# Kernel tuning notes

Hardware: AMD Instinct MI355X
Metric: run time of the kernel (lower is better)

The kernel has to match this reference:

```python
import jax, jax.numpy as jnp
import numpy as np
from jax import lax

BETA = 0.1

def setup_inputs() -> dict:
    key = jax.random.key(0)
    k = jax.random.split(key, 6)
    B, T, H, V = 2, 1024, 1024, 64000
    return {
        "_input": jax.random.normal(k[0], (B, T, H), jnp.float32) * 0.02,
        "weight": jax.random.normal(k[1], (V, H), jnp.float32) * 0.02,
        "attention_mask": (jax.random.uniform(k[2], (B, T)) < 0.9).astype(jnp.float32),
        "rewards": jax.random.normal(k[3], (B,), jnp.float32),
        "ref_input": jax.random.normal(k[4], (B, T, H), jnp.float32) * 0.02,
        "ref_weight": jax.random.normal(k[5], (V, H), jnp.float32) * 0.02,
    }


def _grpo(log_probs, attention_mask, rewards, ref_log_probs, beta):
    # log_probs: [B,T,V]
    chosen = jnp.argmax(log_probs, axis=-1)  # [B,T] int
    tok_lp = jnp.take_along_axis(log_probs, chosen[..., None], axis=-1)[..., 0]  # [B,T]
    ref_tok_lp = lax.stop_gradient(
        jnp.take_along_axis(ref_log_probs, chosen[..., None], axis=-1)[..., 0]
    )
    adv = (rewards - rewards.mean()) / (jnp.std(rewards, ddof=1) + 1e-8)  # [B]
    ratio = jnp.exp(tok_lp - lax.stop_gradient(tok_lp))  # == 1 in fwd, grad-carrying
    policy_loss = -ratio * adv[:, None]
    d = ref_tok_lp - tok_lp
    kl = jnp.exp(d) - d - 1.0
    per_tok = (policy_loss + beta * kl) * attention_mask
    seqlen = jnp.clip(attention_mask.sum(axis=1), 1.0)
    loss = (per_tok.sum(axis=1) / seqlen).mean()
    metrics = (
        tok_lp.mean(),
        jnp.std(tok_lp, ddof=1),
        log_probs.mean(),
        (kl * attention_mask).sum(axis=1).mean() / attention_mask.sum(axis=1).mean(),
    )
    return loss, metrics


def reference(_input, weight, attention_mask, rewards, ref_input, ref_weight):
    logits = jnp.einsum("bth,vh->btv", _input, weight)
    log_probs = jax.nn.log_softmax(logits, axis=-1)
    ref_logits = jnp.einsum("bth,vh->btv", ref_input, ref_weight)
    ref_log_probs = lax.stop_gradient(jax.nn.log_softmax(ref_logits, axis=-1))
    loss, metrics = _grpo(log_probs, attention_mask, rewards, ref_log_probs, BETA)
    return (loss, *metrics)
```

## Files before the change

### kernel.cpp

```cpp
#include <hip/hip_runtime.h>
#include <math.h>

#define GRPO_BETA 0.1f

constexpr int BM = 128;
constexpr int BN = 256;
constexpr int BK = 32;

typedef __attribute__((ext_vector_type(4))) float   f32x4;
typedef __attribute__((ext_vector_type(8))) __bf16  bf16x8;

__device__ __forceinline__ float sexp_fast(float a) { return __expf(fminf(a, 0.f)); }
__device__ __forceinline__ float sexp(float a)      { return expf(fminf(a, 0.f)); }

__device__ __forceinline__ bf16x8 cvt8(float4 a, float4 b) {
  bf16x8 r;
  r[0] = (__bf16)a.x; r[1] = (__bf16)a.y; r[2] = (__bf16)a.z; r[3] = (__bf16)a.w;
  r[4] = (__bf16)b.x; r[5] = (__bf16)b.y; r[6] = (__bf16)b.z; r[7] = (__bf16)b.w;
  return r;
}

__device__ __forceinline__ void bar_lgkm() {
  asm volatile("s_waitcnt lgkmcnt(0)\n\ts_barrier" ::: "memory");
}

__global__ __launch_bounds__(256)
void cvt_bf16_kernel(const float* __restrict__ src, __bf16* __restrict__ dst,
                     long long n8)
{
  long long i = (long long)blockIdx.x * blockDim.x + threadIdx.x;
  const long long stride = (long long)gridDim.x * blockDim.x;
  for (; i < n8; i += stride) {
    const float4 a = *reinterpret_cast<const float4*>(src + i * 8);
    const float4 b = *reinterpret_cast<const float4*>(src + i * 8 + 4);
    *reinterpret_cast<bf16x8*>(dst + i * 8) = cvt8(a, b);
  }
}

template <bool POLICY, bool CVT>
__global__ __launch_bounds__(512, 4)
void mfma_gemm_reduce(const float* __restrict__ Af,
                      const __bf16* __restrict__ Ah,
                      const float* __restrict__ Wf,
                      const __bf16* __restrict__ Wh,
                      float* __restrict__ part,
                      int M, int K, int V, int NC, int NL, int gx)
{
  __shared__ __align__(16) unsigned short lds_a[BM * 64];
  __shared__ __align__(16) unsigned short lds_w[BN * 64];
  __shared__ __align__(16) float4 lds_red[BM * 4];

  const int tid  = threadIdx.x;
  const int lane = tid & 63;
  const int wave = tid >> 6;
  const int wm   = wave >> 2;
  const int wn   = wave & 3;
  const int l15  = lane & 15;
  const int q    = lane >> 4;

  const int nb  = gridDim.x;
  int wl = blockIdx.x;
  if ((nb & 7) == 0) wl = (wl & 7) * (nb >> 3) + (wl >> 3);
  const int bx    = wl % gx;
  const int chunk = wl / gx;
  const int row0  = bx * BM;

  const int t3 = tid & 3;
  const int r4 = tid >> 2;
  const int stw = ((t3 * 16) ^ ((r4 & 7) << 4));
  const int sta = r4 * 128 + stw;

  const int arow = min(row0 + r4, M - 1);
  const int aro  = arow * K + t3 * 8;

  const int swzr  = ((q * 16) ^ ((l15 & 7) << 4));
  const int aoff0 = (wm * 64 + l15) * 128 + swzr;
  const int woff0 = (wn * 64 + l15) * 128 + swzr;

  float rm = -INFINITY, rse = 0.f, rsum = 0.f;
  int   ridx = 0x7fffffff;

  const int NS = K / BK;

  for (int sub = 0; sub < NL; ++sub) {
    const int v0 = (chunk * NL + sub) * BN;
    if (v0 >= V) break;

    int wro[2];
#pragma unroll
    for (int i = 0; i < 2; ++i)
      wro[i] = min(v0 + r4 + 128 * i, V - 1) * K + t3 * 8;

    f32x4 acc[4][4];
#pragma unroll
    for (int i = 0; i < 4; ++i)
#pragma unroll
      for (int j = 0; j < 4; ++j) acc[i][j] = (f32x4){0.f, 0.f, 0.f, 0.f};

    float4 aF[2], wF[2][2];
    bf16x8 aH, wH[2];

    if constexpr (CVT) {
      aF[0] = *reinterpret_cast<const float4*>(Af + aro);
      aF[1] = *reinterpret_cast<const float4*>(Af + aro + 4);
#pragma unroll
      for (int i = 0; i < 2; ++i) {
        wF[i][0] = *reinterpret_cast<const float4*>(Wf + wro[i]);
        wF[i][1] = *reinterpret_cast<const float4*>(Wf + wro[i] + 4);
      }
      *reinterpret_cast<bf16x8*>(reinterpret_cast<char*>(lds_a) + sta) = cvt8(aF[0], aF[1]);
#pragma unroll
      for (int i = 0; i < 2; ++i)
        *reinterpret_cast<bf16x8*>(reinterpret_cast<char*>(lds_w) + (r4 + 128 * i) * 128 + stw) =
            cvt8(wF[i][0], wF[i][1]);
      if (NS > 1) {
        aF[0] = *reinterpret_cast<const float4*>(Af + aro + BK);
        aF[1] = *reinterpret_cast<const float4*>(Af + aro + BK + 4);
#pragma unroll
        for (int i = 0; i < 2; ++i) {
          wF[i][0] = *reinterpret_cast<const float4*>(Wf + wro[i] + BK);
          wF[i][1] = *reinterpret_cast<const float4*>(Wf + wro[i] + BK + 4);
        }
      }
    } else {
      aH = *reinterpret_cast<const bf16x8*>(Ah + aro);
#pragma unroll
      for (int i = 0; i < 2; ++i)
        wH[i] = *reinterpret_cast<const bf16x8*>(Wh + wro[i]);
      *reinterpret_cast<bf16x8*>(reinterpret_cast<char*>(lds_a) + sta) = aH;
#pragma unroll
      for (int i = 0; i < 2; ++i)
        *reinterpret_cast<bf16x8*>(reinterpret_cast<char*>(lds_w) + (r4 + 128 * i) * 128 + stw) = wH[i];
      if (NS > 1) {
        aH = *reinterpret_cast<const bf16x8*>(Ah + aro + BK);
#pragma unroll
        for (int i = 0; i < 2; ++i)
          wH[i] = *reinterpret_cast<const bf16x8*>(Wh + wro[i] + BK);
      }
    }
    bar_lgkm();

    for (int s = 0; s < NS; ++s) {
      const int p = (s & 1) << 6;

      bf16x8 afr[4];
#pragma unroll
      for (int f = 0; f < 4; ++f)
        afr[f] = *reinterpret_cast<const bf16x8*>(
            reinterpret_cast<const char*>(lds_a) + (aoff0 ^ p) + f * 2048);
      __builtin_amdgcn_s_setprio(1);
#pragma unroll
      for (int fn = 0; fn < 4; ++fn) {
        bf16x8 wfr = *reinterpret_cast<const bf16x8*>(
            reinterpret_cast<const char*>(lds_w) + (woff0 ^ p) + fn * 2048);
#pragma unroll
        for (int fm = 0; fm < 4; ++fm)
          acc[fm][fn] = __builtin_amdgcn_mfma_f32_16x16x32_bf16(
              afr[fm], wfr, acc[fm][fn], 0, 0, 0);
      }
      __builtin_amdgcn_s_setprio(0);

      if (s + 1 < NS) {
        const int p1 = ((s + 1) & 1) << 6;
        if constexpr (CVT) {
          *reinterpret_cast<bf16x8*>(reinterpret_cast<char*>(lds_a) + (sta ^ p1)) =
              cvt8(aF[0], aF[1]);
#pragma unroll
          for (int i = 0; i < 2; ++i)
            *reinterpret_cast<bf16x8*>(
                reinterpret_cast<char*>(lds_w) + (((r4 + 128 * i) * 128 + stw) ^ p1)) =
                cvt8(wF[i][0], wF[i][1]);
          if (s + 2 < NS) {
            const int kf = (s + 2) * BK;
            aF[0] = *reinterpret_cast<const float4*>(Af + aro + kf);
            aF[1] = *reinterpret_cast<const float4*>(Af + aro + kf + 4);
#pragma unroll
            for (int i = 0; i < 2; ++i) {
              wF[i][0] = *reinterpret_cast<const float4*>(Wf + wro[i] + kf);
              wF[i][1] = *reinterpret_cast<const float4*>(Wf + wro[i] + kf + 4);
            }
          }
        } else {
          *reinterpret_cast<bf16x8*>(reinterpret_cast<char*>(lds_a) + (sta ^ p1)) = aH;
#pragma unroll
          for (int i = 0; i < 2; ++i)
            *reinterpret_cast<bf16x8*>(
                reinterpret_cast<char*>(lds_w) + (((r4 + 128 * i) * 128 + stw) ^ p1)) = wH[i];
          if (s + 2 < NS) {
            const int kf = (s + 2) * BK;
            aH = *reinterpret_cast<const bf16x8*>(Ah + aro + kf);
#pragma unroll
            for (int i = 0; i < 2; ++i)
              wH[i] = *reinterpret_cast<const bf16x8*>(Wh + wro[i] + kf);
          }
        }
      }
      bar_lgkm();
    }

#pragma unroll
    for (int fm = 0; fm < 4; ++fm) {
#pragma unroll
      for (int reg = 0; reg < 4; ++reg) {
        float lm = -INFINITY;
#pragma unroll
        for (int fn = 0; fn < 4; ++fn) {
          const int v = v0 + wn * 64 + fn * 16 + l15;
          if (v < V) lm = fmaxf(lm, acc[fm][fn][reg]);
        }
#pragma unroll
        for (int d = 1; d < 16; d <<= 1) lm = fmaxf(lm, __shfl_xor(lm, d));
        float se = 0.f, sm = 0.f; int li = 0x7fffffff;
#pragma unroll
        for (int fn = 0; fn < 4; ++fn) {
          const int v = v0 + wn * 64 + fn * 16 + l15;
          if (v < V) {
            const float x = acc[fm][fn][reg];
            se += __expf(x - lm);
            sm += x;
            if (x == lm) li = min(li, v);
          }
        }
#pragma unroll
        for (int d = 1; d < 16; d <<= 1) {
          se += __shfl_xor(se, d);
          sm += __shfl_xor(sm, d);
          li  = min(li, __shfl_xor(li, d));
        }
        if (l15 == 0) {
          const int row = wm * 64 + fm * 16 + q * 4 + reg;
          lds_red[row * 4 + wn] = make_float4(lm, se, sm, __int_as_float(li));
        }
      }
    }
    __syncthreads();

    if (tid < BM) {
      float4 p = lds_red[tid * 4];
      float m = p.x, se = p.y, sm = p.z; int idx = __float_as_int(p.w);
#pragma unroll
      for (int j = 1; j < 4; ++j) {
        const float4 t = lds_red[tid * 4 + j];
        const int ti = __float_as_int(t.w);
        const float nm = fmaxf(m, t.x);
        se = se * sexp_fast(m - nm) + t.y * sexp_fast(t.x - nm);
        sm += t.z;
        if (t.x > m || (t.x == m && ti < idx)) idx = ti;
        m = nm;
      }
      const float nm = fmaxf(rm, m);
      rse = rse * sexp_fast(rm - nm) + se * sexp_fast(m - nm);
      rsum += sm;
      if (m > rm || (m == rm && idx < ridx)) ridx = idx;
      rm = nm;
    }
    __syncthreads();
  }

  if (tid < BM) {
    const int row = row0 + tid;
    if (row < M) {
      if (POLICY) {
        reinterpret_cast<float4*>(part)[(size_t)row * NC + chunk] =
            make_float4(rm, rse, rsum, __int_as_float(ridx));
      } else {
        reinterpret_cast<float2*>(part)[(size_t)row * NC + chunk] =
            make_float2(rm, rse);
      }
    }
  }
}

__global__ __launch_bounds__(256)
void combine_kernel(const float4* __restrict__ partP,
                    const float2* __restrict__ partR,
                    const float* __restrict__ refA,
                    const float* __restrict__ refW,
                    float4* __restrict__ rowtab,
                    int M, int K, int V, int NC)
{
  const int row = blockIdx.x;
  const int tid = threadIdx.x;

  __shared__ float redf[256];
  __shared__ int   redi[256];
  __shared__ float s_M, s_SE, s_SUM, s_Mr, s_SEr, s_dot;
  __shared__ int   s_idx;

  float m = -INFINITY, se = 0.f, sm = 0.f; int idx = 0x7fffffff;
  for (int i = tid; i < NC; i += 256) {
    float4 p = partP[(size_t)row * NC + i];
    int pi = __float_as_int(p.w);
    float nm = fmaxf(m, p.x);
    se = se * sexp(m - nm) + p.y * sexp(p.x - nm);
    if (p.x > m || (p.x == m && pi < idx)) idx = pi;
    m = nm;
    sm += p.z;
  }
  redf[tid] = m; redi[tid] = idx;
  __syncthreads();
  for (int s = 128; s > 0; s >>= 1) {
    if (tid < s) {
      float om = redf[tid + s]; int oi = redi[tid + s];
      if (om > redf[tid] || (om == redf[tid] && oi < redi[tid])) { redf[tid] = om; redi[tid] = oi; }
    }
    __syncthreads();
  }
  if (tid == 0) { s_M = redf[0]; s_idx = redi[0]; }
  __syncthreads();
  const float Mp = s_M; const int chosen = s_idx;

  float contrib = se * sexp(m - Mp);
  __syncthreads();
  redf[tid] = contrib; __syncthreads();
  for (int s = 128; s > 0; s >>= 1) { if (tid < s) redf[tid] += redf[tid + s]; __syncthreads(); }
  if (tid == 0) s_SE = redf[0];
  __syncthreads();
  redf[tid] = sm; __syncthreads();
  for (int s = 128; s > 0; s >>= 1) { if (tid < s) redf[tid] += redf[tid + s]; __syncthreads(); }
  if (tid == 0) s_SUM = redf[0];
  __syncthreads();

  float mr = -INFINITY, ser = 0.f;
  for (int i = tid; i < NC; i += 256) {
    float2 p = partR[(size_t)row * NC + i];
    float nm = fmaxf(mr, p.x);
    ser = ser * sexp(mr - nm) + p.y * sexp(p.x - nm);
    mr = nm;
  }
  redf[tid] = mr; __syncthreads();
  for (int s = 128; s > 0; s >>= 1) { if (tid < s) redf[tid] = fmaxf(redf[tid], redf[tid + s]); __syncthreads(); }
  if (tid == 0) s_Mr = redf[0];
  __syncthreads();
  const float Mr = s_Mr;
  float contribr = ser * sexp(mr - Mr);
  __syncthreads();
  redf[tid] = contribr; __syncthreads();
  for (int s = 128; s > 0; s >>= 1) { if (tid < s) redf[tid] += redf[tid + s]; __syncthreads(); }
  if (tid == 0) s_SEr = redf[0];
  __syncthreads();

  float dp = 0.f;
  const float* ar = refA + (size_t)row * K;
  const float* wr = refW + (size_t)chosen * K;
  for (int j = tid * 4; j < K; j += 256 * 4) {
    float4 x = *reinterpret_cast<const float4*>(ar + j);
    float4 y = *reinterpret_cast<const float4*>(wr + j);
    dp = fmaf(x.x, y.x, dp);
    dp = fmaf(x.y, y.y, dp);
    dp = fmaf(x.z, y.z, dp);
    dp = fmaf(x.w, y.w, dp);
  }
  __syncthreads();
  redf[tid] = dp; __syncthreads();
  for (int s = 128; s > 0; s >>= 1) { if (tid < s) redf[tid] += redf[tid + s]; __syncthreads(); }
  if (tid == 0) s_dot = redf[0];
  __syncthreads();

  if (tid == 0) {
    float lse     = Mp + logf(s_SE);
    float tok     = Mp - lse;
    float ref_lse = Mr + logf(s_SEr);
    float ref_tok = s_dot - ref_lse;
    float d  = ref_tok - tok;
    float kl = expm1f(d) - d;
    float rm3 = s_SUM / (float)V - lse;
    rowtab[row] = make_float4(tok, kl, rm3, 0.f);
  }
}

__global__ __launch_bounds__(256)
void final_kernel(const float4* __restrict__ rowtab,
                  const float* __restrict__ mask,
                  const float* __restrict__ rewards,
                  float* __restrict__ out,
                  int M, int B, int T)
{
  const int tid = threadIdx.x;
  __shared__ float redf[256];
  __shared__ float s_mean, s_m3, s_var;
  __shared__ float s_kl[16], s_cnt[16];

  float st = 0.f, sm3 = 0.f;
  for (int r = tid; r < M; r += 256) {
    float4 v = rowtab[r];
    st += v.x; sm3 += v.z;
  }
  redf[tid] = st; __syncthreads();
  for (int s = 128; s > 0; s >>= 1) { if (tid < s) redf[tid] += redf[tid + s]; __syncthreads(); }
  if (tid == 0) s_mean = redf[0] / (float)M;
  __syncthreads();
  redf[tid] = sm3; __syncthreads();
  for (int s = 128; s > 0; s >>= 1) { if (tid < s) redf[tid] += redf[tid + s]; __syncthreads(); }
  if (tid == 0) s_m3 = redf[0] / (float)M;
  __syncthreads();

  const float mean = s_mean;
  float sv = 0.f;
  for (int r = tid; r < M; r += 256) { float d = rowtab[r].x - mean; sv = fmaf(d, d, sv); }
  __syncthreads();
  redf[tid] = sv; __syncthreads();
  for (int s = 128; s > 0; s >>= 1) { if (tid < s) redf[tid] += redf[tid + s]; __syncthreads(); }
  if (tid == 0) s_var = redf[0];
  __syncthreads();

  const int nb = B < 16 ? B : 16;
  for (int b = 0; b < nb; ++b) {
    float lk = 0.f, lc = 0.f;
    for (int t = tid; t < T; t += 256) {
      int r = b * T + t;
      float mk = mask[r];
      lk = fmaf(rowtab[r].y, mk, lk);
      lc += mk;
    }
    __syncthreads();
    redf[tid] = lk; __syncthreads();
    for (int s = 128; s > 0; s >>= 1) { if (tid < s) redf[tid] += redf[tid + s]; __syncthreads(); }
    if (tid == 0) s_kl[b] = redf[0];
    __syncthreads();
    redf[tid] = lc; __syncthreads();
    for (int s = 128; s > 0; s >>= 1) { if (tid < s) redf[tid] += redf[tid + s]; __syncthreads(); }
    if (tid == 0) s_cnt[b] = redf[0];
    __syncthreads();
  }

  if (tid == 0) {
    float rmean = 0.f;
    for (int b = 0; b < B; ++b) rmean += rewards[b];
    rmean /= (float)B;
    float rv = 0.f;
    for (int b = 0; b < B; ++b) { float d = rewards[b] - rmean; rv += d * d; }
    float rstd = sqrtf(rv / (float)(B > 1 ? B - 1 : 1));

    float loss = 0.f, m4n = 0.f, m4d = 0.f;
    for (int b = 0; b < nb; ++b) {
      float adv  = (rewards[b] - rmean) / (rstd + 1e-8f);
      float cnt  = s_cnt[b];
      float seql = fmaxf(cnt, 1.0f);
      loss += (-adv * cnt + GRPO_BETA * s_kl[b]) / seql;
      m4n += s_kl[b];
      m4d += cnt;
    }
    loss /= (float)B;

    out[0] = loss;
    out[1] = s_mean;
    out[2] = sqrtf(s_var / (float)(M - 1));
    out[3] = s_m3;
    out[4] = m4n / m4d;
  }
}

extern "C" void kernel_launch(void* const* d_in, const int* in_sizes, int n_in,
                              void* d_out, int out_size, void* d_ws, size_t ws_size,
                              hipStream_t stream)
{
  if (n_in < 6) return;
  const float* A       = (const float*)d_in[0];
  const float* W       = (const float*)d_in[1];
  const float* mask    = (const float*)d_in[2];
  const float* rewards = (const float*)d_in[3];
  const float* rA      = (const float*)d_in[4];
  const float* rW      = (const float*)d_in[5];

  const int M = in_sizes[2];
  const int B = in_sizes[3];
  const int T = M / B;
  const int K = in_sizes[0] / M;
  const int V = in_sizes[1] / K;

  const int gx = (M + BM - 1) / BM;

  const size_t aBytes = (size_t)M * K * sizeof(__bf16);
  const size_t wBytes = (size_t)V * K * sizeof(__bf16);
  auto partBytes = [&](int nl) -> size_t {
    int nc = (V + BN * nl - 1) / (BN * nl);
    return (size_t)M * nc * 16 + (size_t)M * nc * 8 + (size_t)M * 16;
  };
  const bool canPrep =
      (K % 8 == 0) && (partBytes(1) + 2 * aBytes + 2 * wBytes <= ws_size);

  int NL = 1;
  if (!canPrep) {
    while (partBytes(NL) > ws_size && NL < 1024) NL <<= 1;
  }
  const int NC = (V + BN * NL - 1) / (BN * NL);

  float* partP  = (float*)d_ws;
  float* partR  = partP + (size_t)M * NC * 4;
  float* rowtab = partR + (size_t)M * NC * 2;

  dim3 g1(gx * NC), b1(512);

  if (canPrep) {
    __bf16* Ab  = (__bf16*)(rowtab + (size_t)M * 4);
    __bf16* rAb = Ab  + (size_t)M * K;
    __bf16* Wb  = rAb + (size_t)M * K;
    __bf16* rWb = Wb  + (size_t)V * K;

    const long long nA8 = (long long)M * K / 8;
    const long long nW8 = (long long)V * K / 8;
    cvt_bf16_kernel<<<dim3(512),  dim3(256), 0, stream>>>(A,  Ab,  nA8);
    cvt_bf16_kernel<<<dim3(512),  dim3(256), 0, stream>>>(rA, rAb, nA8);
    cvt_bf16_kernel<<<dim3(2048), dim3(256), 0, stream>>>(W,  Wb,  nW8);
    cvt_bf16_kernel<<<dim3(2048), dim3(256), 0, stream>>>(rW, rWb, nW8);

    mfma_gemm_reduce<true , false><<<g1, b1, 0, stream>>>(
        nullptr, Ab,  nullptr, Wb,  partP, M, K, V, NC, NL, gx);
    mfma_gemm_reduce<false, false><<<g1, b1, 0, stream>>>(
        nullptr, rAb, nullptr, rWb, partR, M, K, V, NC, NL, gx);
  } else {
    mfma_gemm_reduce<true , true><<<g1, b1, 0, stream>>>(
        A,  nullptr, W,  nullptr, partP, M, K, V, NC, NL, gx);
    mfma_gemm_reduce<false, true><<<g1, b1, 0, stream>>>(
        rA, nullptr, rW, nullptr, partR, M, K, V, NC, NL, gx);
  }

  combine_kernel<<<dim3(M), dim3(256), 0, stream>>>(
      (const float4*)partP, (const float2*)partR, rA, rW, (float4*)rowtab, M, K, V, NC);
  final_kernel<<<dim3(1), dim3(256), 0, stream>>>(
      (const float4*)rowtab, mask, rewards, (float*)d_out, M, B, T);
}
```

Measured before the change: 876.4 us.

## Shrink GEMM tile to 128x128 with 4 waves and specialize reduction paths

Changes the fused GEMM+softmax-reduce tile from 128x256 with 8 waves to 128x128 with 4 waves. Each wave still computes a 64x64 sub-tile, but blocks are smaller and twice as many, with less LDS per block for better occupancy and load balance. Also adds a FULL template that drops vocab bounds checks when V divides BN, skips sum/argmax work in the reference pass, and lets the workspace search pick a larger NL so the bf16 pre-conversion path can still fit. The smaller N tile lowers A-tile reuse per block and doubles the partial-result count the combine kernel must merge.

```diff
diff --git a/kernel.cpp b/kernel.cpp
--- a/kernel.cpp
+++ b/kernel.cpp
@@ -4,7 +4,7 @@
 #define GRPO_BETA 0.1f
 
 constexpr int BM = 128;
-constexpr int BN = 256;
+constexpr int BN = 128;
 constexpr int BK = 32;
 
 typedef __attribute__((ext_vector_type(4))) float   f32x4;
@@ -37,8 +37,8 @@
   }
 }
 
-template <bool POLICY, bool CVT>
-__global__ __launch_bounds__(512, 4)
+template <bool POLICY, bool CVT, bool FULL>
+__global__ __launch_bounds__(256, 4)
 void mfma_gemm_reduce(const float* __restrict__ Af,
                       const __bf16* __restrict__ Ah,
                       const float* __restrict__ Wf,
@@ -48,13 +48,13 @@
 {
   __shared__ __align__(16) unsigned short lds_a[BM * 64];
   __shared__ __align__(16) unsigned short lds_w[BN * 64];
-  __shared__ __align__(16) float4 lds_red[BM * 4];
+  __shared__ __align__(16) float4 lds_red[BM * 2];
 
   const int tid  = threadIdx.x;
   const int lane = tid & 63;
   const int wave = tid >> 6;
-  const int wm   = wave >> 2;
-  const int wn   = wave & 3;
+  const int wm   = wave >> 1;
+  const int wn   = wave & 1;
   const int l15  = lane & 15;
   const int q    = lane >> 4;
 
@@ -68,10 +68,9 @@
   const int t3 = tid & 3;
   const int r4 = tid >> 2;
   const int stw = ((t3 * 16) ^ ((r4 & 7) << 4));
-  const int sta = r4 * 128 + stw;
-
-  const int arow = min(row0 + r4, M - 1);
-  const int aro  = arow * K + t3 * 8;
+  int aro[2];
+#pragma unroll
+  for (int i = 0; i < 2; ++i) aro[i] = min(row0 + r4 + 64 * i, M - 1) * K + t3 * 8;
 
   const int swzr  = ((q * 16) ^ ((l15 & 7) << 4));
   const int aoff0 = (wm * 64 + l15) * 128 + swzr;
@@ -89,7 +88,7 @@
     int wro[2];
 #pragma unroll
     for (int i = 0; i < 2; ++i)
-      wro[i] = min(v0 + r4 + 128 * i, V - 1) * K + t3 * 8;
+      wro[i] = min(v0 + r4 + 64 * i, V - 1) * K + t3 * 8;
 
     f32x4 acc[4][4];
 #pragma unroll
@@ -97,45 +96,50 @@
 #pragma unroll
       for (int j = 0; j < 4; ++j) acc[i][j] = (f32x4){0.f, 0.f, 0.f, 0.f};
 
-    float4 aF[2], wF[2][2];
-    bf16x8 aH, wH[2];
+    float4 aF[2][2], wF[2][2];
+    bf16x8 aH[2], wH[2];
 
     if constexpr (CVT) {
-      aF[0] = *reinterpret_cast<const float4*>(Af + aro);
-      aF[1] = *reinterpret_cast<const float4*>(Af + aro + 4);
 #pragma unroll
       for (int i = 0; i < 2; ++i) {
+        aF[i][0] = *reinterpret_cast<const float4*>(Af + aro[i]);
+        aF[i][1] = *reinterpret_cast<const float4*>(Af + aro[i] + 4);
         wF[i][0] = *reinterpret_cast<const float4*>(Wf + wro[i]);
         wF[i][1] = *reinterpret_cast<const float4*>(Wf + wro[i] + 4);
       }
-      *reinterpret_cast<bf16x8*>(reinterpret_cast<char*>(lds_a) + sta) = cvt8(aF[0], aF[1]);
-#pragma unroll
-      for (int i = 0; i < 2; ++i)
-        *reinterpret_cast<bf16x8*>(reinterpret_cast<char*>(lds_w) + (r4 + 128 * i) * 128 + stw) =
+#pragma unroll
+      for (int i = 0; i < 2; ++i) {
+        *reinterpret_cast<bf16x8*>(reinterpret_cast<char*>(lds_a) + (r4 + 64 * i) * 128 + stw) =
+            cvt8(aF[i][0], aF[i][1]);
+        *reinterpret_cast<bf16x8*>(reinterpret_cast<char*>(lds_w) + (r4 + 64 * i) * 128 + stw) =
             cvt8(wF[i][0], wF[i][1]);
+      }
       if (NS > 1) {
-        aF[0] = *reinterpret_cast<const float4*>(Af + aro + BK);
-        aF[1] = *reinterpret_cast<const float4*>(Af + aro + BK + 4);
 #pragma unroll
         for (int i = 0; i < 2; ++i) {
+          aF[i][0] = *reinterpret_cast<const float4*>(Af + aro[i] + BK);
+          aF[i][1] = *reinterpret_cast<const float4*>(Af + aro[i] + BK + 4);
           wF[i][0] = *reinterpret_cast<const float4*>(Wf + wro[i] + BK);
           wF[i][1] = *reinterpret_cast<const float4*>(Wf + wro[i] + BK + 4);
         }
       }
     } else {
-      aH = *reinterpret_cast<const bf16x8*>(Ah + aro);
-#pragma unroll
-      for (int i = 0; i < 2; ++i)
+#pragma unroll
+      for (int i = 0; i < 2; ++i) {
+        aH[i] = *reinterpret_cast<const bf16x8*>(Ah + aro[i]);
         wH[i] = *reinterpret_cast<const bf16x8*>(Wh + wro[i]);
-      *reinterpret_cast<bf16x8*>(reinterpret_cast<char*>(lds_a) + sta) = aH;
-#pragma unroll
-      for (int i = 0; i < 2; ++i)
-        *reinterpret_cast<bf16x8*>(reinterpret_cast<char*>(lds_w) + (r4 + 128 * i) * 128 + stw) = wH[i];
+      }
+#pragma unroll
+      for (int i = 0; i < 2; ++i) {
+        *reinterpret_cast<bf16x8*>(reinterpret_cast<char*>(lds_a) + (r4 + 64 * i) * 128 + stw) = aH[i];
+        *reinterpret_cast<bf16x8*>(reinterpret_cast<char*>(lds_w) + (r4 + 64 * i) * 128 + stw) = wH[i];
+      }
       if (NS > 1) {
-        aH = *reinterpret_cast<const bf16x8*>(Ah + aro + BK);
-#pragma unroll
-        for (int i = 0; i < 2; ++i)
+#pragma unroll
+        for (int i = 0; i < 2; ++i) {
+          aH[i] = *reinterpret_cast<const bf16x8*>(Ah + aro[i] + BK);
           wH[i] = *reinterpret_cast<const bf16x8*>(Wh + wro[i] + BK);
+        }
       }
     }
     bar_lgkm();
@@ -163,35 +167,40 @@
       if (s + 1 < NS) {
         const int p1 = ((s + 1) & 1) << 6;
         if constexpr (CVT) {
-          *reinterpret_cast<bf16x8*>(reinterpret_cast<char*>(lds_a) + (sta ^ p1)) =
-              cvt8(aF[0], aF[1]);
-#pragma unroll
-          for (int i = 0; i < 2; ++i)
+#pragma unroll
+          for (int i = 0; i < 2; ++i) {
             *reinterpret_cast<bf16x8*>(
-                reinterpret_cast<char*>(lds_w) + (((r4 + 128 * i) * 128 + stw) ^ p1)) =
+                reinterpret_cast<char*>(lds_a) + (((r4 + 64 * i) * 128 + stw) ^ p1)) =
+                cvt8(aF[i][0], aF[i][1]);
+            *reinterpret_cast<bf16x8*>(
+                reinterpret_cast<char*>(lds_w) + (((r4 + 64 * i) * 128 + stw) ^ p1)) =
                 cvt8(wF[i][0], wF[i][1]);
+          }
           if (s + 2 < NS) {
             const int kf = (s + 2) * BK;
-            aF[0] = *reinterpret_cast<const float4*>(Af + aro + kf);
-            aF[1] = *reinterpret_cast<const float4*>(Af + aro + kf + 4);
 #pragma unroll
             for (int i = 0; i < 2; ++i) {
+              aF[i][0] = *reinterpret_cast<const float4*>(Af + aro[i] + kf);
+              aF[i][1] = *reinterpret_cast<const float4*>(Af + aro[i] + kf + 4);
               wF[i][0] = *reinterpret_cast<const float4*>(Wf + wro[i] + kf);
               wF[i][1] = *reinterpret_cast<const float4*>(Wf + wro[i] + kf + 4);
             }
           }
         } else {
-          *reinterpret_cast<bf16x8*>(reinterpret_cast<char*>(lds_a) + (sta ^ p1)) = aH;
-#pragma unroll
-          for (int i = 0; i < 2; ++i)
+#pragma unroll
+          for (int i = 0; i < 2; ++i) {
             *reinterpret_cast<bf16x8*>(
-                reinterpret_cast<char*>(lds_w) + (((r4 + 128 * i) * 128 + stw) ^ p1)) = wH[i];
+                reinterpret_cast<char*>(lds_a) + (((r4 + 64 * i) * 128 + stw) ^ p1)) = aH[i];
+            *reinterpret_cast<bf16x8*>(
+                reinterpret_cast<char*>(lds_w) + (((r4 + 64 * i) * 128 + stw) ^ p1)) = wH[i];
+          }
           if (s + 2 < NS) {
             const int kf = (s + 2) * BK;
-            aH = *reinterpret_cast<const bf16x8*>(Ah + aro + kf);
-#pragma unroll
-            for (int i = 0; i < 2; ++i)
+#pragma unroll
+            for (int i = 0; i < 2; ++i) {
+              aH[i] = *reinterpret_cast<const bf16x8*>(Ah + aro[i] + kf);
               wH[i] = *reinterpret_cast<const bf16x8*>(Wh + wro[i] + kf);
+            }
           }
         }
       }
@@ -205,8 +214,8 @@
         float lm = -INFINITY;
 #pragma unroll
         for (int fn = 0; fn < 4; ++fn) {
-          const int v = v0 + wn * 64 + fn * 16 + l15;
-          if (v < V) lm = fmaxf(lm, acc[fm][fn][reg]);
+          if (FULL || v0 + wn * 64 + fn * 16 + l15 < V)
+            lm = fmaxf(lm, acc[fm][fn][reg]);
         }
 #pragma unroll
         for (int d = 1; d < 16; d <<= 1) lm = fmaxf(lm, __shfl_xor(lm, d));
@@ -214,44 +223,51 @@
 #pragma unroll
         for (int fn = 0; fn < 4; ++fn) {
           const int v = v0 + wn * 64 + fn * 16 + l15;
-          if (v < V) {
+          if (FULL || v < V) {
             const float x = acc[fm][fn][reg];
             se += __expf(x - lm);
-            sm += x;
-            if (x == lm) li = min(li, v);
+            if constexpr (POLICY) {
+              sm += x;
+              if (x == lm) li = min(li, v);
+            }
           }
         }
 #pragma unroll
         for (int d = 1; d < 16; d <<= 1) {
           se += __shfl_xor(se, d);
-          sm += __shfl_xor(sm, d);
-          li  = min(li, __shfl_xor(li, d));
+          if constexpr (POLICY) {
+            sm += __shfl_xor(sm, d);
+            li  = min(li, __shfl_xor(li, d));
+          }
         }
         if (l15 == 0) {
           const int row = wm * 64 + fm * 16 + q * 4 + reg;
-          lds_red[row * 4 + wn] = make_float4(lm, se, sm, __int_as_float(li));
+          lds_red[row * 2 + wn] = make_float4(lm, se, sm, __int_as_float(li));
         }
       }
     }
     __syncthreads();
 
     if (tid < BM) {
-      float4 p = lds_red[tid * 4];
-      float m = p.x, se = p.y, sm = p.z; int idx = __float_as_int(p.w);
-#pragma unroll
-      for (int j = 1; j < 4; ++j) {
-        const float4 t = lds_red[tid * 4 + j];
-        const int ti = __float_as_int(t.w);
-        const float nm = fmaxf(m, t.x);
-        se = se * sexp_fast(m - nm) + t.y * sexp_fast(t.x - nm);
-        sm += t.z;
-        if (t.x > m || (t.x == m && ti < idx)) idx = ti;
+      float4 p0 = lds_red[tid * 2];
+      float4 p1 = lds_red[tid * 2 + 1];
+      float m = p0.x, se = p0.y, sm = p0.z; int idx = __float_as_int(p0.w);
+      {
+        const int ti = __float_as_int(p1.w);
+        const float nm = fmaxf(m, p1.x);
+        se = se * sexp_fast(m - nm) + p1.y * sexp_fast(p1.x - nm);
+        if constexpr (POLICY) {
+          sm += p1.z;
+          if (p1.x > m || (p1.x == m && ti < idx)) idx = ti;
+        }
         m = nm;
       }
       const float nm = fmaxf(rm, m);
       rse = rse * sexp_fast(rm - nm) + se * sexp_fast(m - nm);
-      rsum += sm;
-      if (m > rm || (m == rm && idx < ridx)) ridx = idx;
+      if constexpr (POLICY) {
+        rsum += sm;
+        if (m > rm || (m == rm && idx < ridx)) ridx = idx;
+      }
       rm = nm;
     }
     __syncthreads();
@@ -260,7 +276,7 @@
   if (tid < BM) {
     const int row = row0 + tid;
     if (row < M) {
-      if (POLICY) {
+      if constexpr (POLICY) {
         reinterpret_cast<float4*>(part)[(size_t)row * NC + chunk] =
             make_float4(rm, rse, rsum, __int_as_float(ridx));
       } else {
@@ -470,6 +486,7 @@
   const int V = in_sizes[1] / K;
 
   const int gx = (M + BM - 1) / BM;
+  const bool full = (V % BN) == 0;
 
   const size_t aBytes = (size_t)M * K * sizeof(__bf16);
   const size_t wBytes = (size_t)V * K * sizeof(__bf16);
@@ -477,11 +494,17 @@
     int nc = (V + BN * nl - 1) / (BN * nl);
     return (size_t)M * nc * 16 + (size_t)M * nc * 8 + (size_t)M * 16;
   };
-  const bool canPrep =
-      (K % 8 == 0) && (partBytes(1) + 2 * aBytes + 2 * wBytes <= ws_size);
 
   int NL = 1;
+  bool canPrep = false;
+  if (K % 8 == 0) {
+    for (int nl = 1; nl <= 1024; nl <<= 1) {
+      size_t pb = (partBytes(nl) + 255) & ~(size_t)255;
+      if (pb + 2 * aBytes + 2 * wBytes <= ws_size) { NL = nl; canPrep = true; break; }
+    }
+  }
   if (!canPrep) {
+    NL = 1;
     while (partBytes(NL) > ws_size && NL < 1024) NL <<= 1;
   }
   const int NC = (V + BN * NL - 1) / (BN * NL);
@@ -490,10 +513,11 @@
   float* partR  = partP + (size_t)M * NC * 4;
   float* rowtab = partR + (size_t)M * NC * 2;
 
-  dim3 g1(gx * NC), b1(512);
+  dim3 g1(gx * NC), b1(256);
 
   if (canPrep) {
-    __bf16* Ab  = (__bf16*)(rowtab + (size_t)M * 4);
+    size_t pb = (partBytes(NL) + 255) & ~(size_t)255;
+    __bf16* Ab  = (__bf16*)((char*)d_ws + pb);
     __bf16* rAb = Ab  + (size_t)M * K;
     __bf16* Wb  = rAb + (size_t)M * K;
     __bf16* rWb = Wb  + (size_t)V * K;
@@ -505,15 +529,29 @@
     cvt_bf16_kernel<<<dim3(2048), dim3(256), 0, stream>>>(W,  Wb,  nW8);
     cvt_bf16_kernel<<<dim3(2048), dim3(256), 0, stream>>>(rW, rWb, nW8);
 
-    mfma_gemm_reduce<true , false><<<g1, b1, 0, stream>>>(
-        nullptr, Ab,  nullptr, Wb,  partP, M, K, V, NC, NL, gx);
-    mfma_gemm_reduce<false, false><<<g1, b1, 0, stream>>>(
-        nullptr, rAb, nullptr, rWb, partR, M, K, V, NC, NL, gx);
+    if (full) {
+      mfma_gemm_reduce<true , false, true ><<<g1, b1, 0, stream>>>(
+          nullptr, Ab,  nullptr, Wb,  partP, M, K, V, NC, NL, gx);
+      mfma_gemm_reduce<false, false, true ><<<g1, b1, 0, stream>>>(
+          nullptr, rAb, nullptr, rWb, partR, M, K, V, NC, NL, gx);
+    } else {
+      mfma_gemm_reduce<true , false, false><<<g1, b1, 0, stream>>>(
+          nullptr, Ab,  nullptr, Wb,  partP, M, K, V, NC, NL, gx);
+      mfma_gemm_reduce<false, false, false><<<g1, b1, 0, stream>>>(
+          nullptr, rAb, nullptr, rWb, partR, M, K, V, NC, NL, gx);
+    }
   } else {
-    mfma_gemm_reduce<true , true><<<g1, b1, 0, stream>>>(
-        A,  nullptr, W,  nullptr, partP, M, K, V, NC, NL, gx);
-    mfma_gemm_reduce<false, true><<<g1, b1, 0, stream>>>(
-        rA, nullptr, rW, nullptr, partR, M, K, V, NC, NL, gx);
+    if (full) {
+      mfma_gemm_reduce<true , true , true ><<<g1, b1, 0, stream>>>(
+          A,  nullptr, W,  nullptr, partP, M, K, V, NC, NL, gx);
+      mfma_gemm_reduce<false, true , true ><<<g1, b1, 0, stream>>>(
+          rA, nullptr, rW, nullptr, partR, M, K, V, NC, NL, gx);
+    } else {
+      mfma_gemm_reduce<true , true , false><<<g1, b1, 0, stream>>>(
+          A,  nullptr, W,  nullptr, partP, M, K, V, NC, NL, gx);
+      mfma_gemm_reduce<false, true , false><<<g1, b1, 0, stream>>>(
+          rA, nullptr, rW, nullptr, partR, M, K, V, NC, NL, gx);
+    }
   }
 
   combine_kernel<<<dim3(M), dim3(256), 0, stream>>>(
```

Measured after the change: 898.1 us. +2.5%, slower.

## Fuse policy and reference GEMM-reduce launches into one interleaved grid

Applied to the files above, without the earlier changes.

Merges the two separate GEMM+log-softmax-reduce launches (policy and reference) into a single launch with twice the blocks, with even and odd blocks choosing the policy or reference operands. This removes one launch and the tail drain between the two kernels. Reference blocks now skip the sum/argmax bookkeeping and shuffles, and a FULL template drops the per-column bounds checks when V divides BN. The workspace layout also changes: the bf16 buffers start at a 256-byte-aligned offset, and NL can grow to let the bf16 preconversion path fit in the workspace.

```diff
diff --git a/kernel.cpp b/kernel.cpp
--- a/kernel.cpp
+++ b/kernel.cpp
@@ -37,14 +37,14 @@
   }
 }
 
-template <bool POLICY, bool CVT>
+template <bool CVT, bool FULL>
 __global__ __launch_bounds__(512, 4)
-void mfma_gemm_reduce(const float* __restrict__ Af,
-                      const __bf16* __restrict__ Ah,
-                      const float* __restrict__ Wf,
-                      const __bf16* __restrict__ Wh,
-                      float* __restrict__ part,
-                      int M, int K, int V, int NC, int NL, int gx)
+void fused_gemm_reduce(const float* __restrict__ AfP, const float* __restrict__ WfP,
+                       const float* __restrict__ AfR, const float* __restrict__ WfR,
+                       const __bf16* __restrict__ AhP, const __bf16* __restrict__ WhP,
+                       const __bf16* __restrict__ AhR, const __bf16* __restrict__ WhR,
+                       float* __restrict__ partP, float* __restrict__ partR,
+                       int M, int K, int V, int NC, int NL, int gx)
 {
   __shared__ __align__(16) unsigned short lds_a[BM * 64];
   __shared__ __align__(16) unsigned short lds_w[BN * 64];
@@ -61,9 +61,16 @@
   const int nb  = gridDim.x;
   int wl = blockIdx.x;
   if ((nb & 7) == 0) wl = (wl & 7) * (nb >> 3) + (wl >> 3);
-  const int bx    = wl % gx;
-  const int chunk = wl / gx;
-  const int row0  = bx * BM;
+  const bool isPol = (wl & 1) == 0;
+  const int  w2    = wl >> 1;
+  const int  bx    = w2 % gx;
+  const int  chunk = w2 / gx;
+  const int  row0  = bx * BM;
+
+  const float*  Af = isPol ? AfP : AfR;
+  const float*  Wf = isPol ? WfP : WfR;
+  const __bf16* Ah = isPol ? AhP : AhR;
+  const __bf16* Wh = isPol ? WhP : WhR;
 
   const int t3 = tid & 3;
   const int r4 = tid >> 2;
@@ -205,8 +212,8 @@
         float lm = -INFINITY;
 #pragma unroll
         for (int fn = 0; fn < 4; ++fn) {
-          const int v = v0 + wn * 64 + fn * 16 + l15;
-          if (v < V) lm = fmaxf(lm, acc[fm][fn][reg]);
+          if (FULL || v0 + wn * 64 + fn * 16 + l15 < V)
+            lm = fmaxf(lm, acc[fm][fn][reg]);
         }
 #pragma unroll
         for (int d = 1; d < 16; d <<= 1) lm = fmaxf(lm, __shfl_xor(lm, d));
@@ -214,18 +221,25 @@
 #pragma unroll
         for (int fn = 0; fn < 4; ++fn) {
           const int v = v0 + wn * 64 + fn * 16 + l15;
-          if (v < V) {
+          if (FULL || v < V) {
             const float x = acc[fm][fn][reg];
             se += __expf(x - lm);
-            sm += x;
-            if (x == lm) li = min(li, v);
+            if (isPol) {
+              sm += x;
+              if (x == lm) li = min(li, v);
+            }
           }
         }
-#pragma unroll
-        for (int d = 1; d < 16; d <<= 1) {
-          se += __shfl_xor(se, d);
-          sm += __shfl_xor(sm, d);
-          li  = min(li, __shfl_xor(li, d));
+        if (isPol) {
+#pragma unroll
+          for (int d = 1; d < 16; d <<= 1) {
+            se += __shfl_xor(se, d);
+            sm += __shfl_xor(sm, d);
+            li  = min(li, __shfl_xor(li, d));
+          }
+        } else {
+#pragma unroll
+          for (int d = 1; d < 16; d <<= 1) se += __shfl_xor(se, d);
         }
         if (l15 == 0) {
           const int row = wm * 64 + fm * 16 + q * 4 + reg;
@@ -236,22 +250,26 @@
     __syncthreads();
 
     if (tid < BM) {
-      float4 p = lds_red[tid * 4];
-      float m = p.x, se = p.y, sm = p.z; int idx = __float_as_int(p.w);
+      float4 p0 = lds_red[tid * 4];
+      float m = p0.x, se = p0.y, sm = p0.z; int idx = __float_as_int(p0.w);
 #pragma unroll
       for (int j = 1; j < 4; ++j) {
         const float4 t = lds_red[tid * 4 + j];
         const int ti = __float_as_int(t.w);
         const float nm = fmaxf(m, t.x);
         se = se * sexp_fast(m - nm) + t.y * sexp_fast(t.x - nm);
-        sm += t.z;
-        if (t.x > m || (t.x == m && ti < idx)) idx = ti;
+        if (isPol) {
+          sm += t.z;
+          if (t.x > m || (t.x == m && ti < idx)) idx = ti;
+        }
         m = nm;
       }
       const float nm = fmaxf(rm, m);
       rse = rse * sexp_fast(rm - nm) + se * sexp_fast(m - nm);
-      rsum += sm;
-      if (m > rm || (m == rm && idx < ridx)) ridx = idx;
+      if (isPol) {
+        rsum += sm;
+        if (m > rm || (m == rm && idx < ridx)) ridx = idx;
+      }
       rm = nm;
     }
     __syncthreads();
@@ -260,11 +278,11 @@
   if (tid < BM) {
     const int row = row0 + tid;
     if (row < M) {
-      if (POLICY) {
-        reinterpret_cast<float4*>(part)[(size_t)row * NC + chunk] =
+      if (isPol) {
+        reinterpret_cast<float4*>(partP)[(size_t)row * NC + chunk] =
             make_float4(rm, rse, rsum, __int_as_float(ridx));
       } else {
-        reinterpret_cast<float2*>(part)[(size_t)row * NC + chunk] =
+        reinterpret_cast<float2*>(partR)[(size_t)row * NC + chunk] =
             make_float2(rm, rse);
       }
     }
@@ -470,6 +488,7 @@
   const int V = in_sizes[1] / K;
 
   const int gx = (M + BM - 1) / BM;
+  const bool full = (V % BN) == 0;
 
   const size_t aBytes = (size_t)M * K * sizeof(__bf16);
   const size_t wBytes = (size_t)V * K * sizeof(__bf16);
@@ -477,11 +496,17 @@
     int nc = (V + BN * nl - 1) / (BN * nl);
     return (size_t)M * nc * 16 + (size_t)M * nc * 8 + (size_t)M * 16;
   };
-  const bool canPrep =
-      (K % 8 == 0) && (partBytes(1) + 2 * aBytes + 2 * wBytes <= ws_size);
 
   int NL = 1;
+  bool canPrep = false;
+  if (K % 8 == 0) {
+    for (int nl = 1; nl <= 1024; nl <<= 1) {
+      size_t pb = (partBytes(nl) + 255) & ~(size_t)255;
+      if (pb + 2 * aBytes + 2 * wBytes <= ws_size) { NL = nl; canPrep = true; break; }
+    }
+  }
   if (!canPrep) {
+    NL = 1;
     while (partBytes(NL) > ws_size && NL < 1024) NL <<= 1;
   }
   const int NC = (V + BN * NL - 1) / (BN * NL);
@@ -490,10 +515,11 @@
   float* partR  = partP + (size_t)M * NC * 4;
   float* rowtab = partR + (size_t)M * NC * 2;
 
-  dim3 g1(gx * NC), b1(512);
+  dim3 g1(2 * gx * NC), b1(512);
 
   if (canPrep) {
-    __bf16* Ab  = (__bf16*)(rowtab + (size_t)M * 4);
+    size_t pb = (partBytes(NL) + 255) & ~(size_t)255;
+    __bf16* Ab  = (__bf16*)((char*)d_ws + pb);
     __bf16* rAb = Ab  + (size_t)M * K;
     __bf16* Wb  = rAb + (size_t)M * K;
     __bf16* rWb = Wb  + (size_t)V * K;
@@ -505,15 +531,25 @@
     cvt_bf16_kernel<<<dim3(2048), dim3(256), 0, stream>>>(W,  Wb,  nW8);
     cvt_bf16_kernel<<<dim3(2048), dim3(256), 0, stream>>>(rW, rWb, nW8);
 
-    mfma_gemm_reduce<true , false><<<g1, b1, 0, stream>>>(
-        nullptr, Ab,  nullptr, Wb,  partP, M, K, V, NC, NL, gx);
-    mfma_gemm_reduce<false, false><<<g1, b1, 0, stream>>>(
-        nullptr, rAb, nullptr, rWb, partR, M, K, V, NC, NL, gx);
+    if (full) {
+      fused_gemm_reduce<false, true ><<<g1, b1, 0, stream>>>(
+          nullptr, nullptr, nullptr, nullptr, Ab, Wb, rAb, rWb,
+          partP, partR, M, K, V, NC, NL, gx);
+    } else {
+      fused_gemm_reduce<false, false><<<g1, b1, 0, stream>>>(
+          nullptr, nullptr, nullptr, nullptr, Ab, Wb, rAb, rWb,
+          partP, partR, M, K, V, NC, NL, gx);
+    }
   } else {
-    mfma_gemm_reduce<true , true><<<g1, b1, 0, stream>>>(
-        A,  nullptr, W,  nullptr, partP, M, K, V, NC, NL, gx);
-    mfma_gemm_reduce<false, true><<<g1, b1, 0, stream>>>(
-        rA, nullptr, rW, nullptr, partR, M, K, V, NC, NL, gx);
+    if (full) {
+      fused_gemm_reduce<true , true ><<<g1, b1, 0, stream>>>(
+          A, W, rA, rW, nullptr, nullptr, nullptr, nullptr,
+          partP, partR, M, K, V, NC, NL, gx);
+    } else {
+      fused_gemm_reduce<true , false><<<g1, b1, 0, stream>>>(
+          A, W, rA, rW, nullptr, nullptr, nullptr, nullptr,
+          partP, partR, M, K, V, NC, NL, gx);
+    }
   }
 
   combine_kernel<<<dim3(M), dim3(256), 0, stream>>>(
```

Measured after the change: 878.7 us. No clear change (+0.3%).
